# Optimization experiments

Hardware: AMD Instinct MI355X
Metric: run time of the kernel (lower is better)

Reference implementation:

```python
import jax, jax.numpy as jnp
import numpy as np
import math

T, B, NIN, H, NOUT = 512, 128, 2, 1024, 2
ALPHA = 0.2
SIGMA_REC = math.sqrt(2.0 / ALPHA) * 0.05  # sqrt(2/alpha)*sigma_rec
INITIAL_STD = 0.3


def setup_inputs() -> dict:
    key = jax.random.key(0)
    ks = jax.random.split(key, 7)
    inputs = jax.random.normal(ks[0], (T, B, NIN), dtype=jnp.float32)
    initial_state = jax.random.normal(ks[1], (B, H), dtype=jnp.float32)
    noise = jax.random.normal(ks[2], (T, B, H), dtype=jnp.float32)
    # parameters, initialized as in the torch module
    weight_ih = jax.random.uniform(ks[3], (NIN, H), dtype=jnp.float32, minval=-1.0, maxval=1.0)
    non_diag = jax.random.normal(ks[4], (H, H), dtype=jnp.float32) * (INITIAL_STD / math.sqrt(H))
    eye = jnp.eye(H, dtype=jnp.float32)
    weight_hh = eye * 0.999 + (1.0 - eye) * non_diag
    bias_h = jnp.zeros((1, H), dtype=jnp.float32)
    return {
        'inputs': inputs,
        'initial_state': initial_state,
        'noise': noise,
        'weight_ih': weight_ih,
        'weight_hh': weight_hh,
        'bias_h': bias_h,
    }


def reference(inputs, initial_state, noise, weight_ih, weight_hh, bias_h):
    # Precompute input projection for all steps: [T, B, H]
    inp_proj = jnp.einsum('tbi,ih->tbh', inputs, weight_ih) + bias_h + noise * SIGMA_REC

    def step(state, drive):
        state_new = jnp.matmul(jax.nn.relu(state), weight_hh) + drive
        state = (1.0 - ALPHA) * state + ALPHA * state_new
        return state, state

    _, states = jax.lax.scan(step, initial_state, inp_proj)
    # state_collector includes the initial state: [T+1, B, H]
    return jnp.concatenate([initial_state[None], states], axis=0)
```

## Files before the change

kernel.cpp:

```cpp
#include <hip/hip_runtime.h>

#define T_STEPS 512
#define B_SZ    128
#define H_SZ    1024

typedef __bf16 bf16x8 __attribute__((ext_vector_type(8)));
typedef float  f32x4  __attribute__((ext_vector_type(4)));
typedef float  f32x2  __attribute__((ext_vector_type(2)));

__device__ __forceinline__ void split_bf16(float x, __bf16& hi, __bf16& lo) {
  hi = (__bf16)x;
  lo = (__bf16)(x - (float)hi);
}

__device__ __forceinline__ void store_x2_wt(float* p, f32x2 v) {
  asm volatile("global_store_dwordx2 %0, %1, off sc0 sc1" :: "v"(p), "v"(v) : "memory");
}
__device__ __forceinline__ void wait_vm0() {
  asm volatile("s_waitcnt vmcnt(0)" ::: "memory");
}

__global__ __launch_bounds__(256, 1)
void rnn_scan_kernel(const float* __restrict__ inputs,
                     const float* __restrict__ init_state,
                     const float* __restrict__ noise,
                     const float* __restrict__ wih,
                     const float* __restrict__ whh,
                     const float* __restrict__ bias,
                     float* __restrict__ out,
                     unsigned int* __restrict__ flags) {
  constexpr float kAlpha = 0.2f;
  constexpr float kBeta  = 0.8f;
  constexpr float kSigma = 0.15811388300841897f;

  const int wg   = blockIdx.x;
  const int g    = wg & 7;
  const int s    = wg >> 3;
  const int b0   = g << 4;
  const int j0   = s << 5;
  const int tid  = threadIdx.x;
  const int wave = tid >> 6;
  const int lane = tid & 63;
  const int jn   = lane & 15;
  const int kq   = (lane >> 4) << 3;

  __shared__ float cred[4][2][16][17];

  const int b_l = tid >> 4;
  const int jp  = tid & 15;
  const int jj  = j0 + (jp << 1);
  const int gb  = b0 + b_l;

  const float w0e = wih[jj],        w0o = wih[jj + 1];
  const float w1e = wih[H_SZ + jj], w1o = wih[H_SZ + jj + 1];
  const float be  = bias[jj],       bo  = bias[jj + 1];

  float he = init_state[gb * H_SZ + jj];
  float ho = init_state[gb * H_SZ + jj + 1];
  { f32x2 v; v[0] = he; v[1] = ho; store_x2_wt(&out[gb * H_SZ + jj], v); }

  bf16x8 Bh[8][2], Bl[8][2];
  #pragma unroll
  for (int i = 0; i < 8; ++i) {
    const int kb = (wave << 8) + (i << 5) + kq;
    #pragma unroll
    for (int jt = 0; jt < 2; ++jt) {
      const int jc = j0 + (jt << 4) + jn;
      bf16x8 vh, vl;
      #pragma unroll
      for (int u = 0; u < 8; ++u) {
        const float wv = whh[(kb + u) * H_SZ + jc];
        __bf16 hh, ll; split_bf16(wv, hh, ll);
        vh[u] = hh; vl[u] = ll;
      }
      Bh[i][jt] = vh; Bl[i][jt] = vl;
    }
  }

  wait_vm0();
  __syncthreads();
  if (tid == 0) {
    __hip_atomic_store(&flags[(g << 5) + s], 1u,
                       __ATOMIC_RELAXED, __HIP_MEMORY_SCOPE_AGENT);
  }

  const size_t BH = (size_t)B_SZ * H_SZ;

  for (int t = 0; t < T_STEPS; ++t) {
    f32x2 nz  = *(const f32x2*)&noise[t * BH + gb * H_SZ + jj];
    f32x2 inp = *(const f32x2*)&inputs[(t * B_SZ + gb) * 2];

    {
      const unsigned int target = (unsigned int)(t + 1);
      int spins = 0;
      bool ok;
      do {
        unsigned int v = target;
        if (lane < 32)
          v = __hip_atomic_load(&flags[(g << 5) + lane],
                                __ATOMIC_RELAXED, __HIP_MEMORY_SCOPE_AGENT);
        ok = __all(v >= target);
        if (!ok) { __builtin_amdgcn_s_sleep(1); if (++spins > (1 << 24)) break; }
      } while (!ok);
    }
    asm volatile("" ::: "memory");

    f32x4 acc0 = {0.f, 0.f, 0.f, 0.f}, acc1 = {0.f, 0.f, 0.f, 0.f};
    const float* arow = out + t * BH + (size_t)(b0 + jn) * H_SZ + (wave << 8) + kq;
    #pragma unroll
    for (int i = 0; i < 8; ++i) {
      f32x4 v0 = *(const f32x4*)(arow + (i << 5));
      f32x4 v1 = *(const f32x4*)(arow + (i << 5) + 4);
      bf16x8 ah, al;
      #pragma unroll
      for (int u = 0; u < 4; ++u) {
        const float r0 = fmaxf(v0[u], 0.f);
        const float r1 = fmaxf(v1[u], 0.f);
        __bf16 h0, l0, h1, l1;
        split_bf16(r0, h0, l0); split_bf16(r1, h1, l1);
        ah[u] = h0; al[u] = l0; ah[u + 4] = h1; al[u + 4] = l1;
      }
      acc0 = __builtin_amdgcn_mfma_f32_16x16x32_bf16(ah, Bh[i][0], acc0, 0, 0, 0);
      acc1 = __builtin_amdgcn_mfma_f32_16x16x32_bf16(ah, Bh[i][1], acc1, 0, 0, 0);
      acc0 = __builtin_amdgcn_mfma_f32_16x16x32_bf16(al, Bh[i][0], acc0, 0, 0, 0);
      acc1 = __builtin_amdgcn_mfma_f32_16x16x32_bf16(al, Bh[i][1], acc1, 0, 0, 0);
      acc0 = __builtin_amdgcn_mfma_f32_16x16x32_bf16(ah, Bl[i][0], acc0, 0, 0, 0);
      acc1 = __builtin_amdgcn_mfma_f32_16x16x32_bf16(ah, Bl[i][1], acc1, 0, 0, 0);
    }

    #pragma unroll
    for (int r = 0; r < 4; ++r) {
      const int br = ((lane >> 4) << 2) + r;
      cred[wave][0][br][jn] = acc0[r];
      cred[wave][1][br][jn] = acc1[r];
    }
    __syncthreads();

    const int jt = jp >> 3;
    const int c0 = (jp << 1) & 15;
    const float accE = cred[0][jt][b_l][c0]     + cred[1][jt][b_l][c0]
                     + cred[2][jt][b_l][c0]     + cred[3][jt][b_l][c0];
    const float accO = cred[0][jt][b_l][c0 + 1] + cred[1][jt][b_l][c0 + 1]
                     + cred[2][jt][b_l][c0 + 1] + cred[3][jt][b_l][c0 + 1];
    const float de = fmaf(inp[0], w0e, fmaf(inp[1], w1e, fmaf(kSigma, nz[0], be)));
    const float dq = fmaf(inp[0], w0o, fmaf(inp[1], w1o, fmaf(kSigma, nz[1], bo)));
    he = kBeta * he + kAlpha * (accE + de);
    ho = kBeta * ho + kAlpha * (accO + dq);
    { f32x2 v; v[0] = he; v[1] = ho;
      store_x2_wt(&out[(t + 1) * BH + gb * H_SZ + jj], v); }

    wait_vm0();
    __syncthreads();
    if (tid == 0) {
      __hip_atomic_store(&flags[(g << 5) + s], (unsigned int)(t + 2),
                         __ATOMIC_RELAXED, __HIP_MEMORY_SCOPE_AGENT);
    }
  }
}

extern "C" void kernel_launch(void* const* d_in, const int* in_sizes, int n_in,
                              void* d_out, int out_size, void* d_ws, size_t ws_size,
                              hipStream_t stream) {
  const float* inputs     = (const float*)d_in[0];
  const float* init_state = (const float*)d_in[1];
  const float* noise      = (const float*)d_in[2];
  const float* wih        = (const float*)d_in[3];
  const float* whh        = (const float*)d_in[4];
  const float* bias       = (const float*)d_in[5];
  float* out = (float*)d_out;
  unsigned int* flags = (unsigned int*)d_ws;

  hipMemsetAsync(flags, 0, 256 * sizeof(unsigned int), stream);
  rnn_scan_kernel<<<dim3(256), dim3(256), 0, stream>>>(
      inputs, init_state, noise, wih, whh, bias, out, flags);
}
```

Measured before the change: 2.823 ms.

## Publish pre-split bf16 hi/lo state planes and widen workgroups to 8 waves

Each producer now writes relu(state) already split into bf16 hi and lo planes, double-buffered by step parity, into workspace. Consumers then load those bf16 planes with cache-bypassing loads and feed the MFMAs directly, with no per-step relu and split work. The workgroup grows from 4 to 8 waves, so each wave covers half the K range and the cross-wave LDS reduction sums 8 partials. The cost is extra global stores per element, a workspace-size dependency with an fp32 fallback path, and a deeper reduction.

```diff
diff --git a/kernel.cpp b/kernel.cpp
--- a/kernel.cpp
+++ b/kernel.cpp
@@ -13,14 +13,24 @@
   lo = (__bf16)(x - (float)hi);
 }
 
-__device__ __forceinline__ void store_x2_wt(float* p, f32x2 v) {
-  asm volatile("global_store_dwordx2 %0, %1, off sc0 sc1" :: "v"(p), "v"(v) : "memory");
+__device__ __forceinline__ void store_dword_wt(float* p, float v) {
+  asm volatile("global_store_dword %0, %1, off sc0 sc1" :: "v"(p), "v"(v) : "memory");
+}
+__device__ __forceinline__ void store_short_wt(__bf16* p, __bf16 v) {
+  unsigned int bits = (unsigned int)__builtin_bit_cast(unsigned short, v);
+  asm volatile("global_store_short %0, %1, off sc0 sc1" :: "v"(p), "v"(bits) : "memory");
+}
+__device__ __forceinline__ f32x4 load_x4_wt(const __bf16* p) {
+  f32x4 r;
+  asm volatile("global_load_dwordx4 %0, %1, off sc0 sc1" : "=v"(r) : "v"(p) : "memory");
+  return r;
 }
 __device__ __forceinline__ void wait_vm0() {
   asm volatile("s_waitcnt vmcnt(0)" ::: "memory");
 }
 
-__global__ __launch_bounds__(256, 1)
+template<bool PRESPLIT>
+__global__ __launch_bounds__(512, 2)
 void rnn_scan_kernel(const float* __restrict__ inputs,
                      const float* __restrict__ init_state,
                      const float* __restrict__ noise,
@@ -28,10 +38,12 @@
                      const float* __restrict__ whh,
                      const float* __restrict__ bias,
                      float* __restrict__ out,
-                     unsigned int* __restrict__ flags) {
+                     unsigned int* __restrict__ flags,
+                     __bf16* __restrict__ planes) {
   constexpr float kAlpha = 0.2f;
   constexpr float kBeta  = 0.8f;
   constexpr float kSigma = 0.15811388300841897f;
+  constexpr int   kPlane = B_SZ * H_SZ;
 
   const int wg   = blockIdx.x;
   const int g    = wg & 7;
@@ -44,32 +56,39 @@
   const int jn   = lane & 15;
   const int kq   = (lane >> 4) << 3;
 
-  __shared__ float cred[4][2][16][17];
-
-  const int b_l = tid >> 4;
-  const int jp  = tid & 15;
-  const int jj  = j0 + (jp << 1);
+  __shared__ float cred[8][2][16][17];
+
+  const int b_l = tid >> 5;
+  const int jc  = tid & 31;
+  const int j   = j0 + jc;
   const int gb  = b0 + b_l;
 
-  const float w0e = wih[jj],        w0o = wih[jj + 1];
-  const float w1e = wih[H_SZ + jj], w1o = wih[H_SZ + jj + 1];
-  const float be  = bias[jj],       bo  = bias[jj + 1];
-
-  float he = init_state[gb * H_SZ + jj];
-  float ho = init_state[gb * H_SZ + jj + 1];
-  { f32x2 v; v[0] = he; v[1] = ho; store_x2_wt(&out[gb * H_SZ + jj], v); }
-
-  bf16x8 Bh[8][2], Bl[8][2];
+  const float w0 = wih[j];
+  const float w1 = wih[H_SZ + j];
+  const float bi = bias[j];
+
+  float h = init_state[gb * H_SZ + j];
+  if constexpr (PRESPLIT) {
+    out[gb * H_SZ + j] = h;
+    float r = fmaxf(h, 0.f);
+    __bf16 hh, ll; split_bf16(r, hh, ll);
+    store_short_wt(planes + 0 * kPlane + gb * H_SZ + j, hh);
+    store_short_wt(planes + 1 * kPlane + gb * H_SZ + j, ll);
+  } else {
+    store_dword_wt(&out[gb * H_SZ + j], h);
+  }
+
+  bf16x8 Bh[4][2], Bl[4][2];
   #pragma unroll
-  for (int i = 0; i < 8; ++i) {
-    const int kb = (wave << 8) + (i << 5) + kq;
+  for (int i = 0; i < 4; ++i) {
+    const int kb = (wave << 7) + (i << 5) + kq;
     #pragma unroll
     for (int jt = 0; jt < 2; ++jt) {
-      const int jc = j0 + (jt << 4) + jn;
+      const int jcB = j0 + (jt << 4) + jn;
       bf16x8 vh, vl;
       #pragma unroll
       for (int u = 0; u < 8; ++u) {
-        const float wv = whh[(kb + u) * H_SZ + jc];
+        const float wv = whh[(kb + u) * H_SZ + jcB];
         __bf16 hh, ll; split_bf16(wv, hh, ll);
         vh[u] = hh; vl[u] = ll;
       }
@@ -87,7 +106,7 @@
   const size_t BH = (size_t)B_SZ * H_SZ;
 
   for (int t = 0; t < T_STEPS; ++t) {
-    f32x2 nz  = *(const f32x2*)&noise[t * BH + gb * H_SZ + jj];
+    float nz  = noise[t * BH + gb * H_SZ + j];
     f32x2 inp = *(const f32x2*)&inputs[(t * B_SZ + gb) * 2];
 
     {
@@ -96,8 +115,8 @@
       bool ok;
       do {
         unsigned int v = target;
-        if (lane < 32)
-          v = __hip_atomic_load(&flags[(g << 5) + lane],
+        if (lane < 4)
+          v = __hip_atomic_load(&flags[(g << 5) + (wave << 2) + lane],
                                 __ATOMIC_RELAXED, __HIP_MEMORY_SCOPE_AGENT);
         ok = __all(v >= target);
         if (!ok) { __builtin_amdgcn_s_sleep(1); if (++spins > (1 << 24)) break; }
@@ -106,26 +125,52 @@
     asm volatile("" ::: "memory");
 
     f32x4 acc0 = {0.f, 0.f, 0.f, 0.f}, acc1 = {0.f, 0.f, 0.f, 0.f};
-    const float* arow = out + t * BH + (size_t)(b0 + jn) * H_SZ + (wave << 8) + kq;
-    #pragma unroll
-    for (int i = 0; i < 8; ++i) {
-      f32x4 v0 = *(const f32x4*)(arow + (i << 5));
-      f32x4 v1 = *(const f32x4*)(arow + (i << 5) + 4);
-      bf16x8 ah, al;
-      #pragma unroll
-      for (int u = 0; u < 4; ++u) {
-        const float r0 = fmaxf(v0[u], 0.f);
-        const float r1 = fmaxf(v1[u], 0.f);
-        __bf16 h0, l0, h1, l1;
-        split_bf16(r0, h0, l0); split_bf16(r1, h1, l1);
-        ah[u] = h0; al[u] = l0; ah[u + 4] = h1; al[u + 4] = l1;
-      }
-      acc0 = __builtin_amdgcn_mfma_f32_16x16x32_bf16(ah, Bh[i][0], acc0, 0, 0, 0);
-      acc1 = __builtin_amdgcn_mfma_f32_16x16x32_bf16(ah, Bh[i][1], acc1, 0, 0, 0);
-      acc0 = __builtin_amdgcn_mfma_f32_16x16x32_bf16(al, Bh[i][0], acc0, 0, 0, 0);
-      acc1 = __builtin_amdgcn_mfma_f32_16x16x32_bf16(al, Bh[i][1], acc1, 0, 0, 0);
-      acc0 = __builtin_amdgcn_mfma_f32_16x16x32_bf16(ah, Bl[i][0], acc0, 0, 0, 0);
-      acc1 = __builtin_amdgcn_mfma_f32_16x16x32_bf16(ah, Bl[i][1], acc1, 0, 0, 0);
+
+    if constexpr (PRESPLIT) {
+      const __bf16* hp = planes + (size_t)((t & 1) << 1) * kPlane;
+      const __bf16* lp = hp + kPlane;
+      const int rowoff = (b0 + jn) * H_SZ + (wave << 7) + kq;
+      f32x4 ahr[4], alr[4];
+      #pragma unroll
+      for (int i = 0; i < 4; ++i) {
+        ahr[i] = load_x4_wt(hp + rowoff + (i << 5));
+        alr[i] = load_x4_wt(lp + rowoff + (i << 5));
+      }
+      wait_vm0();
+      __builtin_amdgcn_sched_barrier(0);
+      #pragma unroll
+      for (int i = 0; i < 4; ++i) {
+        bf16x8 ah = __builtin_bit_cast(bf16x8, ahr[i]);
+        bf16x8 al = __builtin_bit_cast(bf16x8, alr[i]);
+        acc0 = __builtin_amdgcn_mfma_f32_16x16x32_bf16(ah, Bh[i][0], acc0, 0, 0, 0);
+        acc1 = __builtin_amdgcn_mfma_f32_16x16x32_bf16(ah, Bh[i][1], acc1, 0, 0, 0);
+        acc0 = __builtin_amdgcn_mfma_f32_16x16x32_bf16(al, Bh[i][0], acc0, 0, 0, 0);
+        acc1 = __builtin_amdgcn_mfma_f32_16x16x32_bf16(al, Bh[i][1], acc1, 0, 0, 0);
+        acc0 = __builtin_amdgcn_mfma_f32_16x16x32_bf16(ah, Bl[i][0], acc0, 0, 0, 0);
+        acc1 = __builtin_amdgcn_mfma_f32_16x16x32_bf16(ah, Bl[i][1], acc1, 0, 0, 0);
+      }
+    } else {
+      const float* arow = out + t * BH + (size_t)(b0 + jn) * H_SZ + (wave << 7) + kq;
+      #pragma unroll
+      for (int i = 0; i < 4; ++i) {
+        f32x4 v0 = *(const f32x4*)(arow + (i << 5));
+        f32x4 v1 = *(const f32x4*)(arow + (i << 5) + 4);
+        bf16x8 ah, al;
+        #pragma unroll
+        for (int u = 0; u < 4; ++u) {
+          const float r0 = fmaxf(v0[u], 0.f);
+          const float r1 = fmaxf(v1[u], 0.f);
+          __bf16 h0, l0, h1, l1;
+          split_bf16(r0, h0, l0); split_bf16(r1, h1, l1);
+          ah[u] = h0; al[u] = l0; ah[u + 4] = h1; al[u + 4] = l1;
+        }
+        acc0 = __builtin_amdgcn_mfma_f32_16x16x32_bf16(ah, Bh[i][0], acc0, 0, 0, 0);
+        acc1 = __builtin_amdgcn_mfma_f32_16x16x32_bf16(ah, Bh[i][1], acc1, 0, 0, 0);
+        acc0 = __builtin_amdgcn_mfma_f32_16x16x32_bf16(al, Bh[i][0], acc0, 0, 0, 0);
+        acc1 = __builtin_amdgcn_mfma_f32_16x16x32_bf16(al, Bh[i][1], acc1, 0, 0, 0);
+        acc0 = __builtin_amdgcn_mfma_f32_16x16x32_bf16(ah, Bl[i][0], acc0, 0, 0, 0);
+        acc1 = __builtin_amdgcn_mfma_f32_16x16x32_bf16(ah, Bl[i][1], acc1, 0, 0, 0);
+      }
     }
 
     #pragma unroll
@@ -136,18 +181,25 @@
     }
     __syncthreads();
 
-    const int jt = jp >> 3;
-    const int c0 = (jp << 1) & 15;
-    const float accE = cred[0][jt][b_l][c0]     + cred[1][jt][b_l][c0]
-                     + cred[2][jt][b_l][c0]     + cred[3][jt][b_l][c0];
-    const float accO = cred[0][jt][b_l][c0 + 1] + cred[1][jt][b_l][c0 + 1]
-                     + cred[2][jt][b_l][c0 + 1] + cred[3][jt][b_l][c0 + 1];
-    const float de = fmaf(inp[0], w0e, fmaf(inp[1], w1e, fmaf(kSigma, nz[0], be)));
-    const float dq = fmaf(inp[0], w0o, fmaf(inp[1], w1o, fmaf(kSigma, nz[1], bo)));
-    he = kBeta * he + kAlpha * (accE + de);
-    ho = kBeta * ho + kAlpha * (accO + dq);
-    { f32x2 v; v[0] = he; v[1] = ho;
-      store_x2_wt(&out[(t + 1) * BH + gb * H_SZ + jj], v); }
+    const int tile = jc >> 4;
+    const int c    = jc & 15;
+    const float a = cred[0][tile][b_l][c] + cred[1][tile][b_l][c]
+                  + cred[2][tile][b_l][c] + cred[3][tile][b_l][c]
+                  + cred[4][tile][b_l][c] + cred[5][tile][b_l][c]
+                  + cred[6][tile][b_l][c] + cred[7][tile][b_l][c];
+    const float d = fmaf(inp[0], w0, fmaf(inp[1], w1, fmaf(kSigma, nz, bi)));
+    h = kBeta * h + kAlpha * (a + d);
+
+    if constexpr (PRESPLIT) {
+      out[(t + 1) * BH + gb * H_SZ + j] = h;
+      float r = fmaxf(h, 0.f);
+      __bf16 hh, ll; split_bf16(r, hh, ll);
+      __bf16* hp = planes + (size_t)(((t + 1) & 1) << 1) * kPlane;
+      store_short_wt(hp + gb * H_SZ + j, hh);
+      store_short_wt(hp + kPlane + gb * H_SZ + j, ll);
+    } else {
+      store_dword_wt(&out[(t + 1) * BH + gb * H_SZ + j], h);
+    }
 
     wait_vm0();
     __syncthreads();
@@ -171,6 +223,14 @@
   unsigned int* flags = (unsigned int*)d_ws;
 
   hipMemsetAsync(flags, 0, 256 * sizeof(unsigned int), stream);
-  rnn_scan_kernel<<<dim3(256), dim3(256), 0, stream>>>(
-      inputs, init_state, noise, wih, whh, bias, out, flags);
-}
+
+  const size_t need = 4096 + (size_t)2 * 2 * B_SZ * H_SZ * sizeof(__bf16);
+  if (ws_size >= need) {
+    __bf16* planes = (__bf16*)((char*)d_ws + 4096);
+    rnn_scan_kernel<true><<<dim3(256), dim3(512), 0, stream>>>(
+        inputs, init_state, noise, wih, whh, bias, out, flags, planes);
+  } else {
+    rnn_scan_kernel<false><<<dim3(256), dim3(512), 0, stream>>>(
+        inputs, init_state, noise, wih, whh, bias, out, flags, (__bf16*)nullptr);
+  }
+}
```

Measured after the change: 2.695 ms. 4.5% less time.
